# Kernel optimization log

Measured on AMD Instinct MI355X. Metric: run time of the kernel, lower is better.

The kernel has to match this reference:

```python
import jax, jax.numpy as jnp
import numpy as np

NL_IN = 0.5      # init kwarg nl_in
CONS = 1e-10     # epsilon added to rates
POISSON_GAIN = 20.0

def setup_inputs() -> dict:
    key = jax.random.key(0)
    k1, k2 = jax.random.split(key)
    shape = (8, 4, 28, 256, 256)  # (bs, c, s, h, w)
    spec_data = jax.random.uniform(k1, shape, dtype=jnp.float32)
    filt = jax.random.uniform(k2, shape, dtype=jnp.float32)
    return {"spec_data": spec_data, "filter": filt}

def reference(spec_data, filter):
    # cap_data = sum over (channel, spectral) dims -> [bs, h, w], then [bs, h, w, 1]
    cap = jnp.sum(spec_data * filter, axis=(1, 2))[..., None]

    # noise synthesis (need_noise=True path)
    poisson_t = jnp.full_like(cap, POISSON_GAIN * NL_IN)
    dark_t = jnp.full_like(cap, 1.0 * NL_IN)
    gauss_t = jnp.full_like(cap, 1.0 * NL_IN)
    peak = cap + CONS

    key = jax.random.key(1)
    kp, kd, kg = jax.random.split(key, 3)
    pnoisy = jax.random.poisson(kp, peak).astype(cap.dtype)
    dnoisy = jax.random.poisson(kd, dark_t).astype(cap.dtype)
    gnoisy = jax.random.normal(kg, cap.shape, dtype=cap.dtype) * gauss_t

    noisy = (pnoisy + dnoisy + gnoisy) * poisson_t / 255.0
    return (noisy, peak, dark_t, gauss_t ** 2)
```

## Files before the change

kernel.cpp:

```cpp
#include <hip/hip_runtime.h>
#include <cstdint>
#include <cstddef>

#pragma clang fp contract(off)

#define N_PIX    524288
#define CSPLANES 112
#define PLANE    65536
#define DCH      48

struct TF2 { uint32_t a, b; };

__host__ __device__ constexpr uint32_t rotl32(uint32_t x, int d) {
  return (x << d) | (x >> (32 - d));
}

__host__ __device__ constexpr TF2 threefry(uint32_t k0, uint32_t k1,
                                           uint32_t c0, uint32_t c1) {
  uint32_t ks2 = k0 ^ k1 ^ 0x1BD11BDAu;
  uint32_t x0 = c0 + k0;
  uint32_t x1 = c1 + k1;
  const int R0[4] = {13, 15, 26, 6};
  const int R1[4] = {17, 29, 16, 24};
  for (int i = 0; i < 4; ++i) { x0 += x1; x1 = rotl32(x1, R0[i]); x1 ^= x0; }
  x0 += k1;  x1 += ks2 + 1u;
  for (int i = 0; i < 4; ++i) { x0 += x1; x1 = rotl32(x1, R1[i]); x1 ^= x0; }
  x0 += ks2; x1 += k0 + 2u;
  for (int i = 0; i < 4; ++i) { x0 += x1; x1 = rotl32(x1, R0[i]); x1 ^= x0; }
  x0 += k0;  x1 += k1 + 3u;
  for (int i = 0; i < 4; ++i) { x0 += x1; x1 = rotl32(x1, R1[i]); x1 ^= x0; }
  x0 += k1;  x1 += ks2 + 4u;
  for (int i = 0; i < 4; ++i) { x0 += x1; x1 = rotl32(x1, R0[i]); x1 ^= x0; }
  x0 += ks2; x1 += k0 + 5u;
  return TF2{x0, x1};
}

struct Chains {
  uint32_t kg0, kg1;
  uint32_t rj0a[DCH], rj0b[DCH], rj1a[DCH], rj1b[DCH];
  uint32_t kda[DCH], kdb[DCH];
  uint32_t kpa[DCH], kpb[DCH];
};

__host__ __device__ constexpr Chains make_chains() {
  Chains c{};
  TF2 kp = threefry(0u, 1u, 0u, 0u);
  TF2 kd = threefry(0u, 1u, 0u, 1u);
  TF2 kg = threefry(0u, 1u, 0u, 2u);
  c.kg0 = kg.a; c.kg1 = kg.b;
  {
    uint32_t a = kp.a, b = kp.b;
    for (int i = 0; i < DCH; ++i) {
      TF2 nk = threefry(a, b, 0u, 0u);
      TF2 s0 = threefry(a, b, 0u, 1u);
      TF2 s1 = threefry(a, b, 0u, 2u);
      c.rj0a[i] = s0.a; c.rj0b[i] = s0.b;
      c.rj1a[i] = s1.a; c.rj1b[i] = s1.b;
      a = nk.a; b = nk.b;
    }
  }
  {
    uint32_t a = kd.a, b = kd.b;
    for (int i = 0; i < DCH; ++i) {
      TF2 nk = threefry(a, b, 0u, 0u);
      TF2 sk = threefry(a, b, 0u, 1u);
      c.kda[i] = sk.a; c.kdb[i] = sk.b;
      a = nk.a; b = nk.b;
    }
  }
  {
    uint32_t a = kp.a, b = kp.b;
    for (int i = 0; i < DCH; ++i) {
      TF2 nk = threefry(a, b, 0u, 0u);
      TF2 sk = threefry(a, b, 0u, 1u);
      c.kpa[i] = sk.a; c.kpb[i] = sk.b;
      a = nk.a; b = nk.b;
    }
  }
  return c;
}

__constant__ Chains G = make_chains();

__device__ inline float u01(uint32_t k0, uint32_t k1, uint32_t j) {
  TF2 r = threefry(k0, k1, 0u, j);
  uint32_t bits = r.a ^ r.b;
  return __uint_as_float((bits >> 9) | 0x3F800000u) - 1.0f;
}

__device__ inline float xla_lgamma(float x_in) {
  float z = x_in - 1.0f;
  float x = 1.0f;
  x = x + 676.520368121885098567009190444019f    / ((z + 0.0f) + 1.0f);
  x = x + (-1259.13921672240287047156078755283f) / ((z + 1.0f) + 1.0f);
  x = x + 771.3234287776530788486528258894f      / ((z + 2.0f) + 1.0f);
  x = x + (-176.61502916214059906584551354f)     / ((z + 3.0f) + 1.0f);
  x = x + 12.507343278686904814458936853f        / ((z + 4.0f) + 1.0f);
  x = x + (-0.13857109526572011689554707f)       / ((z + 5.0f) + 1.0f);
  x = x + 9.984369578019570859563e-6f            / ((z + 6.0f) + 1.0f);
  x = x + 1.50563273514931155834e-7f             / ((z + 7.0f) + 1.0f);
  float t = 7.5f + z;
  float log_t = 2.0149030205422647f + log1pf(z / 7.5f);
  return 0.91893853320467274178f + ((z + 0.5f) - t / log_t) * log_t + logf(x);
}

__device__ inline float xla_erfinv(float xx) {
  float w = -log1pf(-(xx * xx));
  float p;
  if (w < 5.0f) {
    float ww = w - 2.5f;
    p = 2.81022636e-08f;
    p = 3.43273939e-07f + p * ww;
    p = -3.5233877e-06f + p * ww;
    p = -4.39150654e-06f + p * ww;
    p = 0.00021858087f + p * ww;
    p = -0.00125372503f + p * ww;
    p = -0.00417768164f + p * ww;
    p = 0.246640727f + p * ww;
    p = 1.50140941f + p * ww;
  } else {
    float ww = sqrtf(w) - 3.0f;
    p = -0.000200214257f;
    p = 0.000100950558f + p * ww;
    p = 0.00134934322f + p * ww;
    p = -0.00367342844f + p * ww;
    p = 0.00573950773f + p * ww;
    p = -0.0076224613f + p * ww;
    p = 0.00943887047f + p * ww;
    p = 1.00167406f + p * ww;
    p = 2.83297682f + p * ww;
  }
  return p * xx;
}

__device__ inline float xla_normal(uint32_t j) {
  const float lo = -0.999999940395355224609375f;
  float f = u01(G.kg0, G.kg1, j);
  float u = f * (1.0f - lo) + lo;
  u = fmaxf(lo, u);
  return 1.41421356237309504880f * xla_erfinv(u);
}

__device__ inline int knuth_sample(const uint32_t* ka, const uint32_t* kb,
                                   uint32_t j, float lam) {
  const float neg = -lam;
  int k = 0;
  float lp = 0.0f;
  #pragma unroll 1
  for (int i = 0; i < DCH; ++i) {
    if (!(lp > neg)) break;
    ++k;
    float uu = u01(ka[i], kb[i], j);
    lp = lp + logf(uu);
  }
  return k - 1;
}

struct RejC { float lam, loglam, a, b, inva, vr; };

__device__ inline RejC make_rc(float lam) {
  RejC rc;
  rc.lam = lam;
  rc.loglam = logf(lam);
  rc.b = 0.931f + 2.53f * sqrtf(lam);
  rc.a = -0.059f + 0.02483f * rc.b;
  rc.inva = 1.1239f + 1.1328f / (rc.b - 3.4f);
  rc.vr = 0.9277f - 3.6224f / (rc.b - 2.0f);
  return rc;
}

__device__ inline bool rej_step(const RejC& rc, uint32_t j, int i, float* kout) {
  float u = u01(G.rj0a[i], G.rj0b[i], j) - 0.5f;
  float v = u01(G.rj1a[i], G.rj1b[i], j);
  float us = 0.5f - fabsf(u);
  float k = floorf(((2.0f * rc.a / us + rc.b) * u + rc.lam) + 0.43f);
  *kout = k;
  bool accept1 = (us >= 0.07f) && (v <= rc.vr);
  if (accept1) return true;
  bool reject = (k < 0.0f) || ((us < 0.013f) && (v > us));
  if (reject) return false;
  float s = logf(v * rc.inva / (rc.a / (us * us) + rc.b));
  float t = (-rc.lam + k * rc.loglam) - xla_lgamma(k + 1.0f);
  return s <= t;
}

__global__ __launch_bounds__(256, 8) void reduce_kernel(const float* __restrict__ spec,
                                                        const float* __restrict__ filt,
                                                        float* __restrict__ out) {
  const int tid = threadIdx.x;
  const int w = tid >> 6;
  const int l = tid & 63;
  const int pixbase = blockIdx.x << 8;
  const int b_img = pixbase >> 16;
  const int hw = (pixbase & 65535) + (l << 2);
  const size_t base = (size_t)b_img * ((size_t)CSPLANES * PLANE)
                    + (size_t)(w * 28) * PLANE + (size_t)hw;
  const float* sp = spec + base;
  const float* fp = filt + base;

  float ax = 0.f, ay = 0.f, az = 0.f, aw = 0.f;
  #pragma unroll 4
  for (int cs = 0; cs < 28; ++cs) {
    const float4 s = *reinterpret_cast<const float4*>(sp + (size_t)cs * PLANE);
    const float4 f = *reinterpret_cast<const float4*>(fp + (size_t)cs * PLANE);
    ax += s.x * f.x; ay += s.y * f.y; az += s.z * f.z; aw += s.w * f.w;
  }

  __shared__ float part[4][64][4];
  part[w][l][0] = ax; part[w][l][1] = ay; part[w][l][2] = az; part[w][l][3] = aw;
  __syncthreads();

  const int g = tid >> 2, c = tid & 3;
  float c0 = part[0][g][c];
  float c1 = part[1][g][c];
  float c2 = part[2][g][c];
  float c3 = part[3][g][c];
  float cap = ((c0 + c1) + c2) + c3;
  out[N_PIX + pixbase + tid] = cap;
}

__global__ __launch_bounds__(256) void noise_kernel(float* __restrict__ out,
                                                    unsigned* __restrict__ tslot) {
  const uint32_t j = blockIdx.x * 256u + threadIdx.x;
  const float cap = out[N_PIX + j];
  const float peak = cap + 1e-10f;
  out[N_PIX + j] = peak;
  out[j] = (float)knuth_sample(G.kda, G.kdb, j, 0.5f);
  out[2 * N_PIX + j] = xla_normal(j) * 0.5f;

  RejC rc = make_rc(peak);
  unsigned F = DCH;
  #pragma unroll 1
  for (int i = 0; i < DCH; ++i) {
    float kc;
    if (rej_step(rc, j, i, &kc)) { F = (unsigned)(i + 1); break; }
  }

  for (int off = 32; off; off >>= 1) {
    unsigned o = (unsigned)__shfl_down((int)F, off, 64);
    F = F > o ? F : o;
  }
  __shared__ unsigned sred[4];
  if ((threadIdx.x & 63) == 0) sred[threadIdx.x >> 6] = F;
  __syncthreads();
  if (threadIdx.x == 0) {
    unsigned m0 = sred[0] > sred[1] ? sred[0] : sred[1];
    unsigned m1 = sred[2] > sred[3] ? sred[2] : sred[3];
    unsigned m = m0 > m1 ? m0 : m1;
    atomicMax(tslot, m);
  }
}

__global__ __launch_bounds__(256) void resolve_kernel(float* __restrict__ out,
                                                      const unsigned* __restrict__ tslot) {
  const uint32_t j = blockIdx.x * 256u + threadIdx.x;
  const int T = (int)(*tslot);
  const float peak = out[N_PIX + j];
  const float d = out[j];
  const float g = out[2 * N_PIX + j];
  float pv;
  if (peak >= 10.0f) {
    RejC rc = make_rc(peak);
    float kk = -1.0f;
    #pragma unroll 1
    for (int i = T - 1; i >= 0; --i) {
      float kc;
      if (rej_step(rc, j, i, &kc)) { kk = kc; break; }
    }
    pv = (float)(int)kk;
  } else if (peak <= 0.0f) {
    pv = 0.0f;
  } else {
    pv = (float)knuth_sample(G.kpa, G.kpb, j, peak);
  }
  const float noisy = ((pv + d) + g) * 10.0f / 255.0f;
  out[j] = noisy;
  out[2 * N_PIX + j] = 0.5f;
  out[3 * N_PIX + j] = 0.25f;
}

extern "C" void kernel_launch(void* const* d_in, const int* in_sizes, int n_in,
                              void* d_out, int out_size, void* d_ws, size_t ws_size,
                              hipStream_t stream) {
  (void)in_sizes; (void)n_in; (void)out_size; (void)ws_size;
  const float* spec = (const float*)d_in[0];
  const float* filt = (const float*)d_in[1];
  float* out = (float*)d_out;
  unsigned* tslot = (unsigned*)d_ws;
  (void)hipMemsetAsync(d_ws, 0, sizeof(unsigned), stream);
  hipLaunchKernelGGL(reduce_kernel, dim3(N_PIX / 256), dim3(256), 0, stream,
                     spec, filt, out);
  hipLaunchKernelGGL(noise_kernel, dim3(N_PIX / 256), dim3(256), 0, stream,
                     out, tslot);
  hipLaunchKernelGGL(resolve_kernel, dim3(N_PIX / 256), dim3(256), 0, stream,
                     out, tslot);
}
```

Baseline: 505.7 us.

## Fuse reduction, noise and resolve into one persistent kernel with grid barrier

The separate reduce, noise and resolve kernels are replaced by one kernel of 256 blocks of 1024 threads. Each thread now accumulates two pixels over all 112 channel-spectral planes with float2 loads, then draws the noise samples and reaches a grid-wide max-then-barrier through atomics in workspace. The aim is to cut two launches and the intermediate global round-trips of peak, dark and gauss values. In exchange there is one block per CU, narrower loads, and a spin barrier that relies on all blocks being co-resident. The summation order also changes, so results can differ slightly from before.

```diff
diff --git a/kernel.cpp b/kernel.cpp
--- a/kernel.cpp
+++ b/kernel.cpp
@@ -8,6 +8,7 @@
 #define CSPLANES 112
 #define PLANE    65536
 #define DCH      48
+#define NBLK     256
 
 struct TF2 { uint32_t a, b; };
 
@@ -184,99 +185,98 @@
   return s <= t;
 }
 
-__global__ __launch_bounds__(256, 8) void reduce_kernel(const float* __restrict__ spec,
-                                                        const float* __restrict__ filt,
-                                                        float* __restrict__ out) {
-  const int tid = threadIdx.x;
-  const int w = tid >> 6;
-  const int l = tid & 63;
-  const int pixbase = blockIdx.x << 8;
-  const int b_img = pixbase >> 16;
-  const int hw = (pixbase & 65535) + (l << 2);
-  const size_t base = (size_t)b_img * ((size_t)CSPLANES * PLANE)
-                    + (size_t)(w * 28) * PLANE + (size_t)hw;
-  const float* sp = spec + base;
-  const float* fp = filt + base;
-
-  float ax = 0.f, ay = 0.f, az = 0.f, aw = 0.f;
-  #pragma unroll 4
-  for (int cs = 0; cs < 28; ++cs) {
-    const float4 s = *reinterpret_cast<const float4*>(sp + (size_t)cs * PLANE);
-    const float4 f = *reinterpret_cast<const float4*>(fp + (size_t)cs * PLANE);
-    ax += s.x * f.x; ay += s.y * f.y; az += s.z * f.z; aw += s.w * f.w;
-  }
-
-  __shared__ float part[4][64][4];
-  part[w][l][0] = ax; part[w][l][1] = ay; part[w][l][2] = az; part[w][l][3] = aw;
-  __syncthreads();
-
-  const int g = tid >> 2, c = tid & 3;
-  float c0 = part[0][g][c];
-  float c1 = part[1][g][c];
-  float c2 = part[2][g][c];
-  float c3 = part[3][g][c];
-  float cap = ((c0 + c1) + c2) + c3;
-  out[N_PIX + pixbase + tid] = cap;
-}
-
-__global__ __launch_bounds__(256) void noise_kernel(float* __restrict__ out,
-                                                    unsigned* __restrict__ tslot) {
-  const uint32_t j = blockIdx.x * 256u + threadIdx.x;
-  const float cap = out[N_PIX + j];
-  const float peak = cap + 1e-10f;
-  out[N_PIX + j] = peak;
-  out[j] = (float)knuth_sample(G.kda, G.kdb, j, 0.5f);
-  out[2 * N_PIX + j] = xla_normal(j) * 0.5f;
-
-  RejC rc = make_rc(peak);
+__device__ inline unsigned first_accept(const RejC& rc, uint32_t j) {
   unsigned F = DCH;
   #pragma unroll 1
   for (int i = 0; i < DCH; ++i) {
     float kc;
     if (rej_step(rc, j, i, &kc)) { F = (unsigned)(i + 1); break; }
   }
-
-  for (int off = 32; off; off >>= 1) {
-    unsigned o = (unsigned)__shfl_down((int)F, off, 64);
-    F = F > o ? F : o;
-  }
-  __shared__ unsigned sred[4];
-  if ((threadIdx.x & 63) == 0) sred[threadIdx.x >> 6] = F;
-  __syncthreads();
-  if (threadIdx.x == 0) {
-    unsigned m0 = sred[0] > sred[1] ? sred[0] : sred[1];
-    unsigned m1 = sred[2] > sred[3] ? sred[2] : sred[3];
-    unsigned m = m0 > m1 ? m0 : m1;
-    atomicMax(tslot, m);
-  }
-}
-
-__global__ __launch_bounds__(256) void resolve_kernel(float* __restrict__ out,
-                                                      const unsigned* __restrict__ tslot) {
-  const uint32_t j = blockIdx.x * 256u + threadIdx.x;
-  const int T = (int)(*tslot);
-  const float peak = out[N_PIX + j];
-  const float d = out[j];
-  const float g = out[2 * N_PIX + j];
-  float pv;
+  return F;
+}
+
+__device__ inline float resolve_pix(const RejC& rc, float peak, uint32_t j, int T) {
   if (peak >= 10.0f) {
-    RejC rc = make_rc(peak);
     float kk = -1.0f;
     #pragma unroll 1
     for (int i = T - 1; i >= 0; --i) {
       float kc;
       if (rej_step(rc, j, i, &kc)) { kk = kc; break; }
     }
-    pv = (float)(int)kk;
+    return (float)(int)kk;
   } else if (peak <= 0.0f) {
-    pv = 0.0f;
+    return 0.0f;
   } else {
-    pv = (float)knuth_sample(G.kpa, G.kpb, j, peak);
-  }
-  const float noisy = ((pv + d) + g) * 10.0f / 255.0f;
-  out[j] = noisy;
-  out[2 * N_PIX + j] = 0.5f;
-  out[3 * N_PIX + j] = 0.25f;
+    return (float)knuth_sample(G.kpa, G.kpb, j, peak);
+  }
+}
+
+__global__ __launch_bounds__(1024) void fused_kernel(const float* __restrict__ spec,
+                                                     const float* __restrict__ filt,
+                                                     float* __restrict__ out,
+                                                     unsigned* __restrict__ sync) {
+  const int tid = threadIdx.x;
+  const int pixbase = blockIdx.x << 11;
+  const int b_img = pixbase >> 16;
+  const int hw = (pixbase & 65535) + (tid << 1);
+  const size_t base = (size_t)b_img * ((size_t)CSPLANES * PLANE) + (size_t)hw;
+  const float* sp = spec + base;
+  const float* fp = filt + base;
+
+  float a0 = 0.f, a1 = 0.f;
+  #pragma unroll 8
+  for (int cs = 0; cs < CSPLANES; ++cs) {
+    const float2 s = *reinterpret_cast<const float2*>(sp + (size_t)cs * PLANE);
+    const float2 f = *reinterpret_cast<const float2*>(fp + (size_t)cs * PLANE);
+    a0 += s.x * f.x;
+    a1 += s.y * f.y;
+  }
+
+  const uint32_t j0 = (uint32_t)(pixbase + (tid << 1));
+  const uint32_t j1 = j0 + 1u;
+  const float pk0 = a0 + 1e-10f;
+  const float pk1 = a1 + 1e-10f;
+  const float d0 = (float)knuth_sample(G.kda, G.kdb, j0, 0.5f);
+  const float d1 = (float)knuth_sample(G.kda, G.kdb, j1, 0.5f);
+  const float g0 = xla_normal(j0) * 0.5f;
+  const float g1 = xla_normal(j1) * 0.5f;
+  const RejC rc0 = make_rc(pk0);
+  const RejC rc1 = make_rc(pk1);
+  unsigned F0 = first_accept(rc0, j0);
+  unsigned F1 = first_accept(rc1, j1);
+  unsigned F = F0 > F1 ? F0 : F1;
+
+  for (int off = 32; off; off >>= 1) {
+    unsigned o = (unsigned)__shfl_down((int)F, off, 64);
+    F = F > o ? F : o;
+  }
+  __shared__ unsigned sred[16];
+  __shared__ int sT;
+  if ((tid & 63) == 0) sred[tid >> 6] = F;
+  __syncthreads();
+  if (tid == 0) {
+    unsigned m = sred[0];
+    #pragma unroll
+    for (int i = 1; i < 16; ++i) m = m > sred[i] ? m : sred[i];
+    __hip_atomic_fetch_max(&sync[0], m, __ATOMIC_RELAXED, __HIP_MEMORY_SCOPE_AGENT);
+    __hip_atomic_fetch_add(&sync[1], 1u, __ATOMIC_ACQ_REL, __HIP_MEMORY_SCOPE_AGENT);
+    while (__hip_atomic_load(&sync[1], __ATOMIC_ACQUIRE, __HIP_MEMORY_SCOPE_AGENT) < (unsigned)NBLK) {
+      __builtin_amdgcn_s_sleep(8);
+    }
+    sT = (int)__hip_atomic_load(&sync[0], __ATOMIC_RELAXED, __HIP_MEMORY_SCOPE_AGENT);
+  }
+  __syncthreads();
+  const int T = sT;
+
+  const float pv0 = resolve_pix(rc0, pk0, j0, T);
+  const float pv1 = resolve_pix(rc1, pk1, j1, T);
+  const float n0 = ((pv0 + d0) + g0) * 10.0f / 255.0f;
+  const float n1 = ((pv1 + d1) + g1) * 10.0f / 255.0f;
+
+  *reinterpret_cast<float2*>(out + j0)             = make_float2(n0, n1);
+  *reinterpret_cast<float2*>(out + N_PIX + j0)     = make_float2(pk0, pk1);
+  *reinterpret_cast<float2*>(out + 2 * N_PIX + j0) = make_float2(0.5f, 0.5f);
+  *reinterpret_cast<float2*>(out + 3 * N_PIX + j0) = make_float2(0.25f, 0.25f);
 }
 
 extern "C" void kernel_launch(void* const* d_in, const int* in_sizes, int n_in,
@@ -286,12 +286,8 @@
   const float* spec = (const float*)d_in[0];
   const float* filt = (const float*)d_in[1];
   float* out = (float*)d_out;
-  unsigned* tslot = (unsigned*)d_ws;
-  (void)hipMemsetAsync(d_ws, 0, sizeof(unsigned), stream);
-  hipLaunchKernelGGL(reduce_kernel, dim3(N_PIX / 256), dim3(256), 0, stream,
-                     spec, filt, out);
-  hipLaunchKernelGGL(noise_kernel, dim3(N_PIX / 256), dim3(256), 0, stream,
-                     out, tslot);
-  hipLaunchKernelGGL(resolve_kernel, dim3(N_PIX / 256), dim3(256), 0, stream,
-                     out, tslot);
-}
+  unsigned* sync = (unsigned*)d_ws;
+  (void)hipMemsetAsync(d_ws, 0, 2 * sizeof(unsigned), stream);
+  hipLaunchKernelGGL(fused_kernel, dim3(NBLK), dim3(1024), 0, stream,
+                     spec, filt, out, sync);
+}
```

New measurement: 500.8 us. No clear change (-1.0%).
